# Kernel optimization log

Measured on AMD Instinct MI355X. Metric: run time of the kernel, lower is better.

Reference implementation:

```python
import jax, jax.numpy as jnp
import numpy as np

N, IN_DIM = 50000, 1024
E = 100000
NUM_REL = 40
HEADS, OUT_DIM = 4, 200
HID = HEADS * OUT_DIM  # 800
B = 8192
NEG_SLOPE = 0.2


def setup_inputs() -> dict:
    key = jax.random.key(0)
    ks = jax.random.split(key, 12)
    node_emb = jax.random.normal(ks[0], (N, IN_DIM), dtype=jnp.float32)
    # RelGAT learnable params
    W = jax.random.normal(ks[1], (IN_DIM, HID), dtype=jnp.float32) * (1.0 / np.sqrt(IN_DIM))
    bias = jnp.zeros((HID,), dtype=jnp.float32)
    a_src = jax.random.normal(ks[2], (HEADS, OUT_DIM), dtype=jnp.float32) * 0.1
    a_dst = jax.random.normal(ks[3], (HEADS, OUT_DIM), dtype=jnp.float32) * 0.1
    a_rel = jax.random.normal(ks[4], (HEADS, OUT_DIM), dtype=jnp.float32) * 0.1
    rel_feat = jax.random.normal(ks[5], (NUM_REL, HID), dtype=jnp.float32) * 0.1
    # DistMult scorer relation embeddings
    rel_emb = jax.random.normal(ks[6], (NUM_REL, HID), dtype=jnp.float32) * 0.1
    # Graph structure (constants)
    edge_index = jax.random.randint(ks[7], (2, E), 0, N, dtype=jnp.int64)
    edge_type = jax.random.randint(ks[8], (E,), 0, NUM_REL, dtype=jnp.int64)
    # Triple batch
    src_ids = jax.random.randint(ks[9], (B,), 0, N, dtype=jnp.int64)
    rel_ids = jax.random.randint(ks[10], (B,), 0, NUM_REL, dtype=jnp.int64)
    dst_ids = jax.random.randint(ks[11], (B,), 0, N, dtype=jnp.int64)
    return dict(node_emb=node_emb, W=W, bias=bias, a_src=a_src, a_dst=a_dst,
                a_rel=a_rel, rel_feat=rel_feat, rel_emb=rel_emb,
                edge_index=edge_index, edge_type=edge_type,
                src_ids=src_ids, rel_ids=rel_ids, dst_ids=dst_ids)


def _rel_gat(node_emb, W, bias, a_src, a_dst, a_rel, rel_feat, edge_index, edge_type):
    src, dst = edge_index[0], edge_index[1]
    h = (node_emb @ W).reshape(N, HEADS, OUT_DIM)          # [N,H,D]
    hs = h[src]                                            # [E,H,D] gather
    hd = h[dst]                                            # [E,H,D] gather
    r = rel_feat[edge_type].reshape(E, HEADS, OUT_DIM)     # [E,H,D]
    # relation-conditioned attention logits per head
    logits = (jnp.einsum('ehd,hd->eh', hs, a_src)
              + jnp.einsum('ehd,hd->eh', hd, a_dst)
              + jnp.einsum('ehd,hd->eh', r, a_rel))        # [E,H]
    logits = jax.nn.leaky_relu(logits, NEG_SLOPE)
    # segment softmax over incoming edges of each destination node
    seg_max = jax.ops.segment_max(logits, dst, num_segments=N)   # [N,H]
    e = jnp.exp(logits - seg_max[dst])                           # [E,H]
    denom = jax.ops.segment_sum(e, dst, num_segments=N)          # [N,H]
    alpha = e / denom[dst]                                       # [E,H]
    # weighted scatter-aggregate of source messages
    out = jax.ops.segment_sum(alpha[:, :, None] * hs, dst, num_segments=N)  # [N,H,D]
    return out.reshape(N, HID) + bias                            # dropout: eval mode (identity)


def reference(node_emb, W, bias, a_src, a_dst, a_rel, rel_feat, rel_emb,
              edge_index, edge_type, src_ids, rel_ids, dst_ids):
    refined = _rel_gat(node_emb, W, bias, a_src, a_dst, a_rel, rel_feat,
                       edge_index, edge_type)                # [N, HID]
    src_vec = refined[src_ids]                               # [B, HID]
    dst_vec = refined[dst_ids]                               # [B, HID]
    # DistMult: sum(s * r * d)
    scores = jnp.sum(src_vec * rel_emb[rel_ids] * dst_vec, axis=-1)  # [B]
    return scores
```

## Files before the change

kernel.cpp:

```cpp
#include <hip/hip_runtime.h>
#include <hip/hip_bf16.h>
#include <math.h>

#define NN 50000
#define IN_DIM 1024
#define EE 100000
#define NUM_REL 40
#define HEADS 4
#define OUT_D 200
#define HID 800
#define BB 8192
#define SLOT_CAP 16384
#define SRC_CAP 50176

typedef __attribute__((ext_vector_type(8))) short short8;
typedef __attribute__((ext_vector_type(4))) float f32x4;
typedef __attribute__((ext_vector_type(2))) unsigned int u32x2;

__device__ inline unsigned short f2bf(float f) {
    unsigned int u = __float_as_uint(f);
    u += 0x7FFF + ((u >> 16) & 1);
    return (unsigned short)(u >> 16);
}
__device__ inline float bf2f(unsigned short s) {
    return __uint_as_float(((unsigned int)s) << 16);
}
__device__ inline void gl2lds16(const unsigned short* g, unsigned short* l) {
    __builtin_amdgcn_global_load_lds(
        (const __attribute__((address_space(1))) void*)g,
        (__attribute__((address_space(3))) void*)l, 16, 0, 0);
}
__device__ inline u32x2 cvt4(float4 v) {
    u32x2 r;
    asm("v_cvt_pk_bf16_f32 %0, %1, %2" : "=v"(r.x) : "v"(v.x), "v"(v.y));
    asm("v_cvt_pk_bf16_f32 %0, %1, %2" : "=v"(r.y) : "v"(v.z), "v"(v.w));
    return r;
}

__device__ inline int wave_compact(bool won, int* ctr) {
    unsigned long long m = __ballot(won);
    if (!m) return -1;
    int lane = threadIdx.x & 63;
    int leader = __ffsll((long long)m) - 1;
    int base = 0;
    if (lane == leader) base = atomicAdd(ctr, __popcll(m));
    base = __shfl(base, leader, 64);
    return won ? base + __popcll(m & ((1ull << lane) - 1)) : -1;
}

#define INIT_BLOCKS 196
__global__ __launch_bounds__(256) void k_init_wa(int* slot_of_node, int* xrow_of_node,
                                                 int* deg, int* counters,
                                                 const float* W, const float* a_src,
                                                 const float* a_dst, const float* a_rel,
                                                 const float* rel_feat, float* Wa, float* prel) {
    int b = blockIdx.x;
    if (b < INIT_BLOCKS) {
        int i = b * 256 + threadIdx.x;
        if (i < NN) { slot_of_node[i] = -1; xrow_of_node[i] = -1; }
        if (i < SLOT_CAP) deg[i] = 0;
        if (i < 8) counters[i] = 0;
        return;
    }
    int wid = (b - INIT_BLOCKS) * 4 + (threadIdx.x >> 6);
    int lane = threadIdx.x & 63;
    if (wid >= IN_DIM * 8 + NUM_REL * HEADS) return;
    float acc = 0.f;
    int d = lane * 4;
    if (d < OUT_D) {
        const float* row;
        const float* a;
        if (wid < IN_DIM * 8) {
            int k = wid >> 3, c = wid & 7;
            int h = c & 3;
            row = W + (size_t)k * HID + h * OUT_D;
            a = ((c < 4) ? a_src : a_dst) + h * OUT_D;
        } else {
            int j = wid - IN_DIM * 8;
            int r = j >> 2, h = j & 3;
            row = rel_feat + (size_t)r * HID + h * OUT_D;
            a = a_rel + h * OUT_D;
        }
        float4 wv = *(const float4*)(row + d);
        float4 av = *(const float4*)(a + d);
        acc = wv.x * av.x + wv.y * av.y + wv.z * av.z + wv.w * av.w;
    }
    for (int off = 32; off; off >>= 1) acc += __shfl_down(acc, off, 64);
    if (lane == 0) {
        if (wid < IN_DIM * 8) Wa[wid] = acc;
        else prel[wid - IN_DIM * 8] = acc;
    }
}

__global__ void k_build_slots(const int* src_ids, const int* dst_ids,
                              int* slot_of_node, int* counters, int* scorelist) {
    int i = blockIdx.x * 256 + threadIdx.x;
    bool valid = i < 2 * BB;
    int n = 0;
    bool won = false;
    if (valid) {
        n = (i < BB) ? src_ids[i] : dst_ids[i - BB];
        if (slot_of_node[n] == -1)
            won = (atomicCAS(&slot_of_node[n], -1, -2) == -1);
    }
    int s = wave_compact(won, &counters[0]);
    if (won) {
        slot_of_node[n] = s;
        scorelist[s] = n;
    }
}

__global__ void k_edge0(const int* ei, const int* slot_of_node,
                        int* xrow_of_node, int* counters, int* rows, int* deg) {
    int e = blockIdx.x * 256 + threadIdx.x;
    bool valid = e < EE;
    int slot = -1, sn = 0;
    if (valid) {
        int dn = ei[EE + e];
        slot = slot_of_node[dn];
    }
    bool surv = valid && slot >= 0;
    bool won = false;
    if (surv) {
        sn = ei[e];
        if (xrow_of_node[sn] == -1)
            won = (atomicCAS(&xrow_of_node[sn], -1, -2) == -1);
    }
    int t = wave_compact(won, &counters[1]);
    if (won) {
        rows[t] = sn;
        xrow_of_node[sn] = t;
    }
    if (surv) atomicAdd(&deg[slot], 1);
}

__global__ __launch_bounds__(256) void k_tail_scan_wt(const int* scorelist, int* xrow_of_node,
                                                      int* counters, int* rows,
                                                      const int* deg, int* base, int* cursor,
                                                      const float* W, const float* Wa,
                                                      unsigned short* Wt) {
    int t = threadIdx.x;
    if (blockIdx.x == 0) {
        __shared__ int pref[257];
        int s = 0;
        const int4* dv = (const int4*)(deg + t * (SLOT_CAP / 256));
        for (int i = 0; i < SLOT_CAP / 256 / 4; ++i) {
            int4 v = dv[i];
            s += v.x + v.y + v.z + v.w;
        }
        pref[t + 1] = s;
        if (t == 0) pref[0] = 0;
        __syncthreads();
        if (t == 0)
            for (int i = 1; i <= 256; ++i) pref[i] += pref[i - 1];
        __syncthreads();
        int r = pref[t];
        for (int i = 0; i < SLOT_CAP / 256; ++i) {
            int idx = t * (SLOT_CAP / 256) + i;
            base[idx] = r;
            cursor[idx] = r;
            r += deg[idx];
        }
        return;
    }
    if (blockIdx.x <= 64) {
        int i = (blockIdx.x - 1) * 256 + t;
        bool valid = i < counters[0];
        int n = 0;
        bool won = false;
        if (valid) {
            n = scorelist[i];
            won = (xrow_of_node[n] < 0);
        }
        int tt = wave_compact(won, &counters[3]);
        if (won) {
            int xr = counters[1] + tt;
            xrow_of_node[n] = xr;
            rows[xr] = n;
        }
        return;
    }
    int bw = blockIdx.x - 65;
    int n0 = bw >> 5, ks = bw & 31;
    unsigned short* dst = Wt + (size_t)(n0 * 32 + ks) * 512 * 8;
#pragma unroll
    for (int q = 0; q < 2; ++q) {
        int c = q * 256 + t;
        int col = ((c >> 6) << 4) + (c & 15);
        int kc = (c >> 4) & 3;
        int gcol = n0 * 128 + col;
        int kbase = ks * 32 + kc * 8;
        unsigned short o[8];
        if (gcol < HID) {
#pragma unroll
            for (int kj = 0; kj < 8; ++kj) o[kj] = f2bf(W[(size_t)(kbase + kj) * HID + gcol]);
        } else if (gcol < HID + 8) {
#pragma unroll
            for (int kj = 0; kj < 8; ++kj) o[kj] = f2bf(Wa[(size_t)(kbase + kj) * 8 + (gcol - HID)]);
        } else {
#pragma unroll
            for (int kj = 0; kj < 8; ++kj) o[kj] = 0;
        }
        *(short8*)(dst + (size_t)c * 8) = *(short8*)o;
    }
}

#define GBM 128
#define GBN 128

#define ALOADR(K) do {                                                  \
    avA0 = *(const float4*)(ax0 + (size_t)(K) * 32);                    \
    avA1 = *(const float4*)(ax1 + (size_t)(K) * 32);                    \
    avA2 = *(const float4*)(ax2 + (size_t)(K) * 32);                    \
    avA3 = *(const float4*)(ax3 + (size_t)(K) * 32);                    \
} while (0)

#define AWRITE(AS) do {                                                 \
    *(u32x2*)((AS) + acw)        = cvt4(avA0);                          \
    *(u32x2*)((AS) + acw + 1024) = cvt4(avA1);                          \
    *(u32x2*)((AS) + acw + 2048) = cvt4(avA2);                          \
    *(u32x2*)((AS) + acw + 3072) = cvt4(avA3);                          \
} while (0)

#define BSTAGE(BS, KS) do {                                             \
    gl2lds16(bsrc + ((size_t)(KS) * 512 + t) * 8,       (BS) + (size_t)t * 8);       \
    gl2lds16(bsrc + ((size_t)(KS) * 512 + 256 + t) * 8, (BS) + (size_t)(256 + t) * 8); \
} while (0)

#define COMPUTE(AS, BS) do {                                            \
    short8 af[4], bf4[4];                                               \
    _Pragma("unroll")                                                   \
    for (int i = 0; i < 4; ++i)                                         \
        af[i] = *(const short8*)&(AS)[(size_t)((ga + i) * 64 + lane) * 8]; \
    _Pragma("unroll")                                                   \
    for (int j = 0; j < 4; ++j)                                         \
        bf4[j] = *(const short8*)&(BS)[(size_t)((gb + j) * 64 + lane) * 8]; \
    __builtin_amdgcn_s_setprio(1);                                      \
    _Pragma("unroll")                                                   \
    for (int i = 0; i < 4; ++i)                                         \
        _Pragma("unroll")                                               \
        for (int j = 0; j < 4; ++j)                                     \
            acc[i][j] = __builtin_amdgcn_mfma_f32_16x16x32_bf16(af[i], bf4[j], acc[i][j], 0, 0, 0); \
    __builtin_amdgcn_s_setprio(0);                                      \
} while (0)

#define WAIT2   asm volatile("s_waitcnt vmcnt(2)" ::: "memory")
#define WAIT0   asm volatile("s_waitcnt vmcnt(0)" ::: "memory")
#define PUBBAR  asm volatile("s_waitcnt lgkmcnt(0)\n\ts_barrier" ::: "memory")

__global__ __launch_bounds__(256, 3) void k_hgemm(const float* x, const int* rows,
                                                  const unsigned short* Wt,
                                                  const int* counters, unsigned short* h_src,
                                                  float* sS, float* sD) {
    int nsrc = counters[1];
    int nneed = nsrc + counters[3];
    int lin = blockIdx.x + 7 * blockIdx.y;
    int g = lin / 56, r = lin % 56;
    int rowb = g * 8 + (r & 7);
    int colb = r >> 3;
    int col0 = colb * GBN;
    int row0 = rowb * GBM;
    int rowlim = (colb == 6) ? nneed : nsrc;
    if (row0 >= rowlim) return;
    __shared__ unsigned short As0[4096], As1[4096];
    __shared__ unsigned short Bs0[4096], Bs1[4096], Bs2[4096];
    int t = threadIdx.x;
    int r0 = t >> 3;
    int fo = (t & 7) * 4;
    int lim = nneed - 1;
    const float* ax0 = x + (size_t)rows[min(row0 + r0,      lim)] * IN_DIM + fo;
    const float* ax1 = x + (size_t)rows[min(row0 + r0 + 32, lim)] * IN_DIM + fo;
    const float* ax2 = x + (size_t)rows[min(row0 + r0 + 64, lim)] * IN_DIM + fo;
    const float* ax3 = x + (size_t)rows[min(row0 + r0 + 96, lim)] * IN_DIM + fo;
    int kc = (t & 7) >> 1, half = t & 1;
    int acw = (((r0 >> 4) * 64) + kc * 16 + (r0 & 15)) * 8 + half * 4;
    const unsigned short* bsrc = Wt + (size_t)colb * 32 * 512 * 8;
    int w = t >> 6, lane = t & 63;
    int ga = (w >> 1) * 4, gb = (w & 1) * 4;
    int wr = (w >> 1) * 64, wc = (w & 1) * 64;
    int fm = lane & 15, fq = lane >> 4;
    float4 avA0, avA1, avA2, avA3;
    f32x4 acc[4][4] = {};
    unsigned short *bA = Bs0, *bB = Bs1, *bC = Bs2;
    unsigned short *aC = As0, *aW = As1;
    BSTAGE(bA, 0);
    ALOADR(0);
    BSTAGE(bB, 1);
    WAIT2;
    AWRITE(aC);
    ALOADR(1);
    PUBBAR;
#pragma unroll 1
    for (int k = 0; k < 30; ++k) {
        BSTAGE(bC, k + 2);
        COMPUTE(aC, bA);
        WAIT2;
        AWRITE(aW);
        ALOADR(k + 2);
        PUBBAR;
        unsigned short* tb = bA; bA = bB; bB = bC; bC = tb;
        unsigned short* ta = aC; aC = aW; aW = ta;
    }
    COMPUTE(aC, bA);
    WAIT0;
    AWRITE(aW);
    PUBBAR;
    COMPUTE(aW, bB);
#pragma unroll
    for (int i = 0; i < 4; ++i) {
#pragma unroll
        for (int j = 0; j < 4; ++j) {
            int gcol = col0 + wc + j * 16 + fm;
            if (gcol >= HID + 8) continue;
#pragma unroll
            for (int rr = 0; rr < 4; ++rr) {
                int grow = row0 + wr + i * 16 + fq * 4 + rr;
                float v = acc[i][j][rr];
                if (gcol < HID) {
                    if (grow < nsrc) h_src[(size_t)grow * HID + gcol] = f2bf(v);
                } else if (grow < nneed) {
                    int c = gcol - HID;
                    if (c < 4) sS[grow * 4 + c] = v;
                    else sD[grow * 4 + (c - 4)] = v;
                }
            }
        }
    }
}

__global__ void k_place(const int* ei, const int* etype, const int* slot_of_node,
                        const int* xrow_of_node, int* cursor,
                        const float* sS, const float* sD, const float* prel,
                        float* clogit, int* tlist) {
    int e = blockIdx.x * 256 + threadIdx.x;
    if (e >= EE) return;
    int dn = ei[EE + e];
    int slot = slot_of_node[dn];
    if (slot < 0) return;
    int sn = ei[e];
    int r = etype[e];
    int xs = xrow_of_node[sn];
    int xd = xrow_of_node[dn];
    int pos = atomicAdd(&cursor[slot], 1);
    tlist[pos] = xs;
    float4 lg;
    float* lp = (float*)&lg;
#pragma unroll
    for (int h = 0; h < 4; ++h) {
        float v = sS[xs * 4 + h] + sD[xd * 4 + h] + prel[r * 4 + h];
        lp[h] = v > 0.f ? v : 0.2f * v;
    }
    *(float4*)&clogit[(size_t)pos * 4] = lg;
}

__global__ __launch_bounds__(256) void k_aggregate(const int* counters, const int* base,
                                                   const int* deg, const int* tlist,
                                                   const float* clogit,
                                                   const unsigned short* h_src, const float* bias,
                                                   float* refined) {
    int b = blockIdx.x;
    if (b >= counters[0]) return;
    int beg = base[b], d = deg[b];
    __shared__ float m4[4], den4[4];
    __shared__ float alpha[64][4];
    __shared__ int tsl[64];
    int t = threadIdx.x;
    if (t < 4) {
        float m = -3e38f;
        for (int j = 0; j < d; ++j)
            m = fmaxf(m, clogit[(size_t)(beg + j) * 4 + t]);
        float s = 0.f;
        for (int j = 0; j < d; ++j)
            s += expf(clogit[(size_t)(beg + j) * 4 + t] - m);
        m4[t] = m;
        den4[t] = s;
    }
    __syncthreads();
    int head = t / 50;
    float4 acc = {0.f, 0.f, 0.f, 0.f};
    for (int j0 = 0; j0 < d; j0 += 64) {
        int nc = min(64, d - j0);
        if (t < nc * 4) {
            int j = t >> 2, h = t & 3;
            alpha[j][h] = expf(clogit[(size_t)(beg + j0 + j) * 4 + h] - m4[h]) / den4[h];
            if (h == 0) tsl[j] = tlist[beg + j0 + j];
        }
        __syncthreads();
        if (t < 200) {
            for (int j = 0; j < nc; ++j) {
                float a = alpha[j][head];
                ushort4 hv = *(const ushort4*)(h_src + (size_t)tsl[j] * HID + t * 4);
                acc.x += a * bf2f(hv.x);
                acc.y += a * bf2f(hv.y);
                acc.z += a * bf2f(hv.z);
                acc.w += a * bf2f(hv.w);
            }
        }
        __syncthreads();
    }
    if (t < 200) {
        float4 bv = *(const float4*)(bias + t * 4);
        float4 o = {acc.x + bv.x, acc.y + bv.y, acc.z + bv.z, acc.w + bv.w};
        *(float4*)(refined + (size_t)b * HID + t * 4) = o;
    }
}

__global__ __launch_bounds__(256) void k_score(const int* src_ids, const int* rel_ids,
                                               const int* dst_ids, const int* slot_of_node,
                                               const float* rel_emb, const float* refined,
                                               float* out) {
    int gid = blockIdx.x * 256 + threadIdx.x;
    int b = gid >> 6;
    int lane = threadIdx.x & 63;
    if (b >= BB) return;
    int ss = slot_of_node[src_ids[b]];
    int ds = slot_of_node[dst_ids[b]];
    int r = rel_ids[b];
    const float* sv = refined + (size_t)ss * HID;
    const float* dv = refined + (size_t)ds * HID;
    const float* rv = rel_emb + (size_t)r * HID;
    float acc = 0.f;
    for (int c4 = lane; c4 < 200; c4 += 64) {
        float4 s = *(const float4*)(sv + c4 * 4);
        float4 dq = *(const float4*)(dv + c4 * 4);
        float4 rr = *(const float4*)(rv + c4 * 4);
        acc += s.x * rr.x * dq.x + s.y * rr.y * dq.y + s.z * rr.z * dq.z + s.w * rr.w * dq.w;
    }
    for (int off = 32; off; off >>= 1) acc += __shfl_down(acc, off, 64);
    if (lane == 0) out[b] = acc;
}

extern "C" void kernel_launch(void* const* d_in, const int* in_sizes, int n_in,
                              void* d_out, int out_size, void* d_ws, size_t ws_size,
                              hipStream_t stream) {
    const float* node_emb = (const float*)d_in[0];
    const float* W        = (const float*)d_in[1];
    const float* bias     = (const float*)d_in[2];
    const float* a_src    = (const float*)d_in[3];
    const float* a_dst    = (const float*)d_in[4];
    const float* a_rel    = (const float*)d_in[5];
    const float* rel_feat = (const float*)d_in[6];
    const float* rel_emb  = (const float*)d_in[7];
    const int* edge_index = (const int*)d_in[8];
    const int* edge_type  = (const int*)d_in[9];
    const int* src_ids    = (const int*)d_in[10];
    const int* rel_ids    = (const int*)d_in[11];
    const int* dst_ids    = (const int*)d_in[12];
    float* out = (float*)d_out;

    char* w = (char*)d_ws;
    auto alloc = [&](size_t bytes) -> void* {
        void* p = (void*)w;
        w += (bytes + 255) & ~(size_t)255;
        return p;
    };
    int* slot_of_node = (int*)alloc((size_t)NN * 4);
    int* xrow_of_node = (int*)alloc((size_t)NN * 4);
    int* scorelist    = (int*)alloc((size_t)SLOT_CAP * 4);
    int* rows         = (int*)alloc((size_t)NN * 4);
    int* counters     = (int*)alloc(256);
    int* deg          = (int*)alloc((size_t)SLOT_CAP * 4);
    int* base         = (int*)alloc((size_t)SLOT_CAP * 4);
    int* cursor       = (int*)alloc((size_t)SLOT_CAP * 4);
    int* tlist        = (int*)alloc((size_t)EE * 4);
    float* clogit = (float*)alloc((size_t)EE * 4 * 4);
    float* sS     = (float*)alloc((size_t)SRC_CAP * 4 * 4);
    float* sD     = (float*)alloc((size_t)SRC_CAP * 4 * 4);
    float* Wa     = (float*)alloc((size_t)IN_DIM * 8 * 4);
    float* prel   = (float*)alloc((size_t)NUM_REL * 4 * 4);
    unsigned short* Wt    = (unsigned short*)alloc((size_t)7 * 32 * 512 * 8 * 2);
    unsigned short* h_src = (unsigned short*)alloc((size_t)SRC_CAP * HID * 2);
    float* refined = (float*)alloc((size_t)SLOT_CAP * HID * 4);

    int wa_blocks = (IN_DIM * 8 + NUM_REL * HEADS + 3) / 4;
    k_init_wa<<<INIT_BLOCKS + wa_blocks, 256, 0, stream>>>(
        slot_of_node, xrow_of_node, deg, counters,
        W, a_src, a_dst, a_rel, rel_feat, Wa, prel);
    k_build_slots<<<(2 * BB + 255) / 256, 256, 0, stream>>>(src_ids, dst_ids, slot_of_node,
                                                            counters, scorelist);
    k_edge0<<<(EE + 255) / 256, 256, 0, stream>>>(edge_index, slot_of_node,
                                                  xrow_of_node, counters, rows, deg);
    k_tail_scan_wt<<<65 + 224, 256, 0, stream>>>(scorelist, xrow_of_node, counters,
                                                 rows, deg, base, cursor, W, Wa, Wt);
    dim3 ggrid(7, 392);
    k_hgemm<<<ggrid, 256, 0, stream>>>(node_emb, rows, Wt, counters, h_src, sS, sD);
    k_place<<<(EE + 255) / 256, 256, 0, stream>>>(edge_index, edge_type, slot_of_node,
                                                  xrow_of_node, cursor, sS, sD, prel,
                                                  clogit, tlist);
    k_aggregate<<<SLOT_CAP, 256, 0, stream>>>(counters, base, deg, tlist,
                                              clogit, h_src, bias, refined);
    k_score<<<(BB * 64 + 255) / 256, 256, 0, stream>>>(src_ids, rel_ids, dst_ids,
                                                       slot_of_node, rel_emb, refined, out);
}
```

Measured before the change: 461.0 us.

## Use 512-thread GEMM blocks with K=64 stages and batch four slots per aggregate block

The projection GEMM now runs 512 threads (8 waves, 2x4 wave grid, each wave computing a 64x32 tile) and doubles the K depth per pipeline stage to 64. That halves the loop trip count and barrier count, and the A prefetch is moved ahead of compute with adjusted vmcnt waits. Shared memory per block doubles, and launch bounds now request 4 blocks of 512 threads, which may limit residency. Separately, the aggregate kernel processes four destination slots per block in a loop, cutting the block count by a factor of four to reduce launch and scheduling overhead.

```diff
diff --git a/kernel.cpp b/kernel.cpp
--- a/kernel.cpp
+++ b/kernel.cpp
@@ -208,47 +208,51 @@
 #define GBM 128
 #define GBN 128
 
-#define ALOADR(K) do {                                                  \
-    avA0 = *(const float4*)(ax0 + (size_t)(K) * 32);                    \
-    avA1 = *(const float4*)(ax1 + (size_t)(K) * 32);                    \
-    avA2 = *(const float4*)(ax2 + (size_t)(K) * 32);                    \
-    avA3 = *(const float4*)(ax3 + (size_t)(K) * 32);                    \
+#define AGLOAD(K) do {                                                  \
+    fA0 = *(const float4*)(axA + (size_t)(K) * 64);                     \
+    fA1 = *(const float4*)(axA + (size_t)(K) * 64 + 32);                \
+    fA2 = *(const float4*)(axB + (size_t)(K) * 64);                     \
+    fA3 = *(const float4*)(axB + (size_t)(K) * 64 + 32);                \
 } while (0)
 
 #define AWRITE(AS) do {                                                 \
-    *(u32x2*)((AS) + acw)        = cvt4(avA0);                          \
-    *(u32x2*)((AS) + acw + 1024) = cvt4(avA1);                          \
-    *(u32x2*)((AS) + acw + 2048) = cvt4(avA2);                          \
-    *(u32x2*)((AS) + acw + 3072) = cvt4(avA3);                          \
+    *(u32x2*)((AS) + wA)            = cvt4(fA0);                        \
+    *(u32x2*)((AS) + wA + 512 * 8)  = cvt4(fA1);                        \
+    *(u32x2*)((AS) + wB)            = cvt4(fA2);                        \
+    *(u32x2*)((AS) + wB + 512 * 8)  = cvt4(fA3);                        \
 } while (0)
 
-#define BSTAGE(BS, KS) do {                                             \
-    gl2lds16(bsrc + ((size_t)(KS) * 512 + t) * 8,       (BS) + (size_t)t * 8);       \
-    gl2lds16(bsrc + ((size_t)(KS) * 512 + 256 + t) * 8, (BS) + (size_t)(256 + t) * 8); \
+#define BSTAGE(BS, R) do {                                              \
+    gl2lds16(bsrc + ((size_t)(2 * (R)) * 512 + t) * 8,     (BS) + (size_t)t * 8); \
+    gl2lds16(bsrc + ((size_t)(2 * (R) + 1) * 512 + t) * 8, (BS) + (size_t)(512 + t) * 8); \
 } while (0)
 
 #define COMPUTE(AS, BS) do {                                            \
-    short8 af[4], bf4[4];                                               \
     _Pragma("unroll")                                                   \
-    for (int i = 0; i < 4; ++i)                                         \
-        af[i] = *(const short8*)&(AS)[(size_t)((ga + i) * 64 + lane) * 8]; \
-    _Pragma("unroll")                                                   \
-    for (int j = 0; j < 4; ++j)                                         \
-        bf4[j] = *(const short8*)&(BS)[(size_t)((gb + j) * 64 + lane) * 8]; \
-    __builtin_amdgcn_s_setprio(1);                                      \
-    _Pragma("unroll")                                                   \
-    for (int i = 0; i < 4; ++i)                                         \
+    for (int s = 0; s < 2; ++s) {                                       \
+        short8 af[4], bf2r[2];                                          \
         _Pragma("unroll")                                               \
-        for (int j = 0; j < 4; ++j)                                     \
-            acc[i][j] = __builtin_amdgcn_mfma_f32_16x16x32_bf16(af[i], bf4[j], acc[i][j], 0, 0, 0); \
-    __builtin_amdgcn_s_setprio(0);                                      \
+        for (int i = 0; i < 4; ++i)                                     \
+            af[i] = *(const short8*)&(AS)[(size_t)(s * 512 + (ga + i) * 64 + lane) * 8]; \
+        _Pragma("unroll")                                               \
+        for (int j = 0; j < 2; ++j)                                     \
+            bf2r[j] = *(const short8*)&(BS)[(size_t)(s * 512 + (gb + j) * 64 + lane) * 8]; \
+        __builtin_amdgcn_s_setprio(1);                                  \
+        _Pragma("unroll")                                               \
+        for (int i = 0; i < 4; ++i)                                     \
+            _Pragma("unroll")                                           \
+            for (int j = 0; j < 2; ++j)                                 \
+                acc[i][j] = __builtin_amdgcn_mfma_f32_16x16x32_bf16(af[i], bf2r[j], acc[i][j], 0, 0, 0); \
+        __builtin_amdgcn_s_setprio(0);                                  \
+    }                                                                   \
 } while (0)
 
-#define WAIT2   asm volatile("s_waitcnt vmcnt(2)" ::: "memory")
+#define WAIT6   asm volatile("s_waitcnt vmcnt(6)" ::: "memory")
+#define WAIT4   asm volatile("s_waitcnt vmcnt(4)" ::: "memory")
 #define WAIT0   asm volatile("s_waitcnt vmcnt(0)" ::: "memory")
 #define PUBBAR  asm volatile("s_waitcnt lgkmcnt(0)\n\ts_barrier" ::: "memory")
 
-__global__ __launch_bounds__(256, 3) void k_hgemm(const float* x, const int* rows,
+__global__ __launch_bounds__(512, 4) void k_hgemm(const float* x, const int* rows,
                                                   const unsigned short* Wt,
                                                   const int* counters, unsigned short* h_src,
                                                   float* sS, float* sD) {
@@ -262,54 +266,54 @@
     int row0 = rowb * GBM;
     int rowlim = (colb == 6) ? nneed : nsrc;
     if (row0 >= rowlim) return;
-    __shared__ unsigned short As0[4096], As1[4096];
-    __shared__ unsigned short Bs0[4096], Bs1[4096], Bs2[4096];
+    __shared__ unsigned short As0[8192], As1[8192];
+    __shared__ unsigned short Bs0[8192], Bs1[8192], Bs2[8192];
     int t = threadIdx.x;
-    int r0 = t >> 3;
-    int fo = (t & 7) * 4;
+    int rA = t >> 3, jo = (t & 7) * 4;
     int lim = nneed - 1;
-    const float* ax0 = x + (size_t)rows[min(row0 + r0,      lim)] * IN_DIM + fo;
-    const float* ax1 = x + (size_t)rows[min(row0 + r0 + 32, lim)] * IN_DIM + fo;
-    const float* ax2 = x + (size_t)rows[min(row0 + r0 + 64, lim)] * IN_DIM + fo;
-    const float* ax3 = x + (size_t)rows[min(row0 + r0 + 96, lim)] * IN_DIM + fo;
-    int kc = (t & 7) >> 1, half = t & 1;
-    int acw = (((r0 >> 4) * 64) + kc * 16 + (r0 & 15)) * 8 + half * 4;
+    const float* axA = x + (size_t)rows[min(row0 + rA,      lim)] * IN_DIM + jo;
+    const float* axB = x + (size_t)rows[min(row0 + rA + 64, lim)] * IN_DIM + jo;
+    int jj = t & 7;
+    int wA = (((rA >> 4) << 6) + ((jj >> 1) << 4) + (rA & 15)) * 8 + (jj & 1) * 4;
+    int rB = rA + 64;
+    int wB = (((rB >> 4) << 6) + ((jj >> 1) << 4) + (rB & 15)) * 8 + (jj & 1) * 4;
     const unsigned short* bsrc = Wt + (size_t)colb * 32 * 512 * 8;
     int w = t >> 6, lane = t & 63;
-    int ga = (w >> 1) * 4, gb = (w & 1) * 4;
-    int wr = (w >> 1) * 64, wc = (w & 1) * 64;
+    int ga = (w >> 2) * 4, gb = (w & 3) * 2;
+    int wr = (w >> 2) * 64, wc = (w & 3) * 32;
     int fm = lane & 15, fq = lane >> 4;
-    float4 avA0, avA1, avA2, avA3;
-    f32x4 acc[4][4] = {};
+    float4 fA0, fA1, fA2, fA3;
+    f32x4 acc[4][2] = {};
+    unsigned short *aC = As0, *aW = As1;
     unsigned short *bA = Bs0, *bB = Bs1, *bC = Bs2;
-    unsigned short *aC = As0, *aW = As1;
+    AGLOAD(0);
     BSTAGE(bA, 0);
-    ALOADR(0);
     BSTAGE(bB, 1);
-    WAIT2;
+    WAIT4;
     AWRITE(aC);
-    ALOADR(1);
+    AGLOAD(1);
+    WAIT0;
     PUBBAR;
 #pragma unroll 1
-    for (int k = 0; k < 30; ++k) {
+    for (int k = 0; k < 14; ++k) {
+        AWRITE(aW);
+        AGLOAD(k + 2);
         BSTAGE(bC, k + 2);
         COMPUTE(aC, bA);
-        WAIT2;
-        AWRITE(aW);
-        ALOADR(k + 2);
+        WAIT6;
         PUBBAR;
+        unsigned short* ta = aC; aC = aW; aW = ta;
         unsigned short* tb = bA; bA = bB; bB = bC; bC = tb;
-        unsigned short* ta = aC; aC = aW; aW = ta;
-    }
+    }
+    AWRITE(aW);
     COMPUTE(aC, bA);
     WAIT0;
-    AWRITE(aW);
     PUBBAR;
     COMPUTE(aW, bB);
 #pragma unroll
     for (int i = 0; i < 4; ++i) {
 #pragma unroll
-        for (int j = 0; j < 4; ++j) {
+        for (int j = 0; j < 2; ++j) {
             int gcol = col0 + wc + j * 16 + fm;
             if (gcol >= HID + 8) continue;
 #pragma unroll
@@ -358,50 +362,55 @@
                                                    const float* clogit,
                                                    const unsigned short* h_src, const float* bias,
                                                    float* refined) {
-    int b = blockIdx.x;
-    if (b >= counters[0]) return;
-    int beg = base[b], d = deg[b];
     __shared__ float m4[4], den4[4];
     __shared__ float alpha[64][4];
     __shared__ int tsl[64];
     int t = threadIdx.x;
-    if (t < 4) {
-        float m = -3e38f;
-        for (int j = 0; j < d; ++j)
-            m = fmaxf(m, clogit[(size_t)(beg + j) * 4 + t]);
-        float s = 0.f;
-        for (int j = 0; j < d; ++j)
-            s += expf(clogit[(size_t)(beg + j) * 4 + t] - m);
-        m4[t] = m;
-        den4[t] = s;
-    }
-    __syncthreads();
-    int head = t / 50;
-    float4 acc = {0.f, 0.f, 0.f, 0.f};
-    for (int j0 = 0; j0 < d; j0 += 64) {
-        int nc = min(64, d - j0);
-        if (t < nc * 4) {
-            int j = t >> 2, h = t & 3;
-            alpha[j][h] = expf(clogit[(size_t)(beg + j0 + j) * 4 + h] - m4[h]) / den4[h];
-            if (h == 0) tsl[j] = tlist[beg + j0 + j];
-        }
+    int nslot = counters[0];
+#pragma unroll 1
+    for (int s = 0; s < 4; ++s) {
+        int b = blockIdx.x * 4 + s;
         __syncthreads();
+        if (b >= nslot) continue;
+        int beg = base[b], d = deg[b];
+        if (t < 4) {
+            float m = -3e38f;
+            for (int j = 0; j < d; ++j)
+                m = fmaxf(m, clogit[(size_t)(beg + j) * 4 + t]);
+            float ss = 0.f;
+            for (int j = 0; j < d; ++j)
+                ss += expf(clogit[(size_t)(beg + j) * 4 + t] - m);
+            m4[t] = m;
+            den4[t] = ss;
+        }
+        __syncthreads();
+        int head = t / 50;
+        float4 acc = {0.f, 0.f, 0.f, 0.f};
+        for (int j0 = 0; j0 < d; j0 += 64) {
+            int nc = min(64, d - j0);
+            if (t < nc * 4) {
+                int j = t >> 2, h = t & 3;
+                alpha[j][h] = expf(clogit[(size_t)(beg + j0 + j) * 4 + h] - m4[h]) / den4[h];
+                if (h == 0) tsl[j] = tlist[beg + j0 + j];
+            }
+            __syncthreads();
+            if (t < 200) {
+                for (int j = 0; j < nc; ++j) {
+                    float a = alpha[j][head];
+                    ushort4 hv = *(const ushort4*)(h_src + (size_t)tsl[j] * HID + t * 4);
+                    acc.x += a * bf2f(hv.x);
+                    acc.y += a * bf2f(hv.y);
+                    acc.z += a * bf2f(hv.z);
+                    acc.w += a * bf2f(hv.w);
+                }
+            }
+            __syncthreads();
+        }
         if (t < 200) {
-            for (int j = 0; j < nc; ++j) {
-                float a = alpha[j][head];
-                ushort4 hv = *(const ushort4*)(h_src + (size_t)tsl[j] * HID + t * 4);
-                acc.x += a * bf2f(hv.x);
-                acc.y += a * bf2f(hv.y);
-                acc.z += a * bf2f(hv.z);
-                acc.w += a * bf2f(hv.w);
-            }
-        }
-        __syncthreads();
-    }
-    if (t < 200) {
-        float4 bv = *(const float4*)(bias + t * 4);
-        float4 o = {acc.x + bv.x, acc.y + bv.y, acc.z + bv.z, acc.w + bv.w};
-        *(float4*)(refined + (size_t)b * HID + t * 4) = o;
+            float4 bv = *(const float4*)(bias + t * 4);
+            float4 o = {acc.x + bv.x, acc.y + bv.y, acc.z + bv.z, acc.w + bv.w};
+            *(float4*)(refined + (size_t)b * HID + t * 4) = o;
+        }
     }
 }
 
@@ -483,12 +492,12 @@
     k_tail_scan_wt<<<65 + 224, 256, 0, stream>>>(scorelist, xrow_of_node, counters,
                                                  rows, deg, base, cursor, W, Wa, Wt);
     dim3 ggrid(7, 392);
-    k_hgemm<<<ggrid, 256, 0, stream>>>(node_emb, rows, Wt, counters, h_src, sS, sD);
+    k_hgemm<<<ggrid, 512, 0, stream>>>(node_emb, rows, Wt, counters, h_src, sS, sD);
     k_place<<<(EE + 255) / 256, 256, 0, stream>>>(edge_index, edge_type, slot_of_node,
                                                   xrow_of_node, cursor, sS, sD, prel,
                                                   clogit, tlist);
-    k_aggregate<<<SLOT_CAP, 256, 0, stream>>>(counters, base, deg, tlist,
-                                              clogit, h_src, bias, refined);
+    k_aggregate<<<SLOT_CAP / 4, 256, 0, stream>>>(counters, base, deg, tlist,
+                                                  clogit, h_src, bias, refined);
     k_score<<<(BB * 64 + 255) / 256, 256, 0, stream>>>(src_ids, rel_ids, dst_ids,
                                                        slot_of_node, rel_emb, refined, out);
 }
```

Measured after the change: 449.5 us. -2.5%, faster.
